# Kernel tuning notes

Hardware: AMD Instinct MI355X
Metric: run time of the kernel (lower is better)

The kernel has to match this reference:

```python
import jax, jax.numpy as jnp
import numpy as np

STRIDE = 4; R = 3; LEVELS = 4; LAT = 128; RES = (384, 512); D_IN = 1110; T_EMB = 50

def _sincos_1d(d, pos):
    omega = np.arange(d // 2, dtype=np.float64) / (d / 2.0)
    omega = 1.0 / 10000 ** omega
    out = pos.reshape(-1)[:, None] * omega[None, :]
    return np.concatenate([np.sin(out), np.cos(out)], axis=1).astype(np.float32)

def _support(coords, r):
    # coords [B, N, 3] (t, x, y) -> [B, N, 2r+1, 2r+1, 3]; offsets only in x,y
    d = jnp.linspace(-r, r, 2 * r + 1, dtype=jnp.float32)
    g0, g1 = jnp.meshgrid(d, d, indexing='ij')
    delta = jnp.stack([jnp.zeros_like(g0), g0, g1], axis=-1)
    return coords[:, :, None, None, :] + delta[None, None]

def _trilinear(fmap, coords):
    # fmap [B, C, Dd, H, W]; coords [B, M, 3] = (t, x, y); border padding, align_corners=True
    B, C, Dd, H, W = fmap.shape
    t = jnp.clip(coords[..., 0], 0.0, Dd - 1)
    x = jnp.clip(coords[..., 1], 0.0, W - 1)
    y = jnp.clip(coords[..., 2], 0.0, H - 1)
    t0f = jnp.floor(t); x0f = jnp.floor(x); y0f = jnp.floor(y)
    wt = (t - t0f)[:, None, :]; wx = (x - x0f)[:, None, :]; wy = (y - y0f)[:, None, :]
    t0 = t0f.astype(jnp.int32); t1 = jnp.minimum(t0 + 1, Dd - 1)
    x0 = x0f.astype(jnp.int32); x1 = jnp.minimum(x0 + 1, W - 1)
    y0 = y0f.astype(jnp.int32); y1 = jnp.minimum(y0 + 1, H - 1)
    flat = fmap.reshape(B, C, Dd * H * W)
    def g(ti, yi, xi):
        idx = (ti * H + yi) * W + xi
        return jnp.take_along_axis(flat, idx[:, None, :], axis=2)  # [B, C, M]
    def bilin(ti):
        v00 = g(ti, y0, x0); v01 = g(ti, y0, x1); v10 = g(ti, y1, x0); v11 = g(ti, y1, x1)
        return (v00 * (1 - wy) * (1 - wx) + v01 * (1 - wy) * wx
                + v10 * wy * (1 - wx) + v11 * wy * wx)
    return bilin(t0) * (1 - wt) + bilin(t1) * wt

def _posenc(x, min_deg, max_deg):
    scales = 2.0 ** jnp.arange(min_deg, max_deg, dtype=jnp.float32)
    xb = (x[..., None, :] * scales[:, None]).reshape(x.shape[:-1] + (-1,))
    ff = jnp.sin(jnp.concatenate([xb, xb + 0.5 * jnp.pi], axis=-1))
    return jnp.concatenate([x, ff], axis=-1)

def _interp_time(emb, t):
    T0 = emb.shape[1]
    if t == T0:
        return emb
    sc = T0 / float(t)
    j = jnp.clip((jnp.arange(t, dtype=jnp.float32) + 0.5) * sc - 0.5, 0.0, T0 - 1)
    j0 = jnp.floor(j).astype(jnp.int32); j1 = jnp.minimum(j0 + 1, T0 - 1)
    w = (j - j0)[None, :, None]
    return emb[:, j0] * (1 - w) + emb[:, j1] * w

def setup_inputs():
    key = jax.random.key(0)
    ks = jax.random.split(key, 10)
    B, T, N, H, W = 1, 16, 128, RES[0], RES[1]
    video = jax.random.uniform(ks[0], (B, T, 3, H, W), jnp.float32) * 255.0
    fr = jax.random.randint(ks[1], (B, N), 0, T).astype(jnp.float32)
    cx = jax.random.uniform(ks[2], (B, N), jnp.float32) * (W - 1)
    cy = jax.random.uniform(ks[3], (B, N), jnp.float32) * (H - 1)
    queries = jnp.stack([fr, cx, cy], axis=-1)
    s = 0.02
    return {
        'video': video,
        'queries': queries,
        'fnet_w': jax.random.normal(ks[4], (LAT, 3, 4, 4), jnp.float32) * s,
        'fnet_b': jnp.zeros((LAT,), jnp.float32),
        'fc1_w': jax.random.normal(ks[5], (2401, 384), jnp.float32) * s,
        'fc1_b': jnp.zeros((384,), jnp.float32),
        'fc2_w': jax.random.normal(ks[6], (384, 256), jnp.float32) * s,
        'fc2_b': jnp.zeros((256,), jnp.float32),
        'up_w1': jax.random.normal(ks[7], (D_IN, 384), jnp.float32) * s,
        'up_b1': jnp.zeros((384,), jnp.float32),
        'up_w2': jax.random.normal(ks[8], (384, 4), jnp.float32) * s,
        'up_b2': jnp.zeros((4,), jnp.float32),
        'time_emb': jnp.asarray(_sincos_1d(D_IN, np.linspace(0, T_EMB - 1, T_EMB))[None]),
        'iters': 4,
    }

def reference(video, queries, fnet_w, fnet_b, fc1_w, fc1_b, fc2_w, fc2_b,
              up_w1, up_b1, up_w2, up_b2, time_emb, iters):
    B, T, C, H, W = video.shape
    N = queries.shape[1]
    video = 2.0 * (video / 255.0) - 1.0
    qf = queries[:, :, 0]            # queried frames (used as float t coordinate)
    qc = queries[..., 1:3] / STRIDE  # (x, y) in feature-map coords
    # --- encoder (stand-in conv), L2-normalize over channels ---
    f = jax.lax.conv_general_dilated(video.reshape(B * T, C, H, W), fnet_w,
                                     (STRIDE, STRIDE), 'VALID') + fnet_b[None, :, None, None]
    f = f / jnp.sqrt(jnp.maximum(jnp.sum(f * f, axis=1, keepdims=True), 1e-12))
    fmaps = f.reshape(B, T, LAT, H // STRIDE, W // STRIDE)
    # --- avg-pool pyramid ---
    pyr = [fmaps]
    for _ in range(LEVELS - 1):
        p = pyr[-1]
        pyr.append(p.reshape(B, T, LAT, p.shape[-2] // 2, 2, p.shape[-1] // 2, 2).mean(axis=(4, 6)))
    r = R; rr = 2 * r + 1
    # --- track support features per level: [B, N, rr, rr, LAT] ---
    tfs = []
    for i in range(LEVELS):
        sc = jnp.concatenate([qf[..., None], qc / (2.0 ** i)], axis=-1)  # [B,N,3]
        sp = _support(sc, r).reshape(B, N * rr * rr, 3)
        feat = _trilinear(pyr[i].transpose(0, 2, 1, 3, 4), sp)  # [B, LAT, N*rr*rr]
        tfs.append(feat.reshape(B, LAT, N, rr, rr).transpose(0, 2, 3, 4, 1))
    vis = jnp.zeros((B, T, N), jnp.float32)
    conf = jnp.zeros((B, T, N), jnp.float32)
    coords = jnp.broadcast_to(qc.reshape(B, 1, N, 2), (B, T, N, 2)).astype(jnp.float32)
    scale = jnp.array([RES[1], RES[0]], jnp.float32) / STRIDE
    te = _interp_time(time_emb, T)  # [1, T, D_IN]
    for _ in range(iters):
        coords = jax.lax.stop_gradient(coords)
        cflat = coords.reshape(B * T, N, 2)
        embs = []
        for i in range(LEVELS):
            fm = pyr[i]
            Hi, Wi = fm.shape[-2], fm.shape[-1]
            sc = jnp.concatenate([jnp.zeros_like(cflat[..., :1]), cflat / (2.0 ** i)], axis=-1)
            sp = _support(sc, r).reshape(B * T, N * rr * rr, 3)
            cf = _trilinear(fm.reshape(B * T, LAT, 1, Hi, Wi), sp)  # [B*T, LAT, N*rr*rr]
            cf = cf.reshape(B, T, LAT, N, rr, rr).transpose(0, 1, 3, 4, 5, 2)  # [B,T,N,rr,rr,LAT]
            cv = jnp.einsum('btnhwc,bnijc->btnhwij', cf, tfs[i]).reshape(B * T * N, rr * rr * rr * rr)
            e = jax.nn.gelu(cv @ fc1_w + fc1_b, approximate=False) @ fc2_w + fc2_b
            embs.append(e)
        corr = jnp.concatenate(embs, axis=-1).reshape(B, T, N, -1)  # [B,T,N,1024]
        rf = jnp.pad(coords[:, :-1] - coords[:, 1:], ((0, 0), (0, 1), (0, 0), (0, 0))) / scale
        rb = jnp.pad(coords[:, 1:] - coords[:, :-1], ((0, 0), (1, 0), (0, 0), (0, 0))) / scale
        pe = _posenc(jnp.concatenate([rf, rb], axis=-1), 0, 10)  # [B,T,N,84]
        x = jnp.concatenate([vis[..., None], conf[..., None], corr, pe], axis=-1)  # [B,T,N,1110]
        x = x.transpose(0, 2, 1, 3) + te[None]  # [B,N,T,1110]
        delta = jax.nn.gelu(x @ up_w1 + up_b1, approximate=False) @ up_w2 + up_b2  # [B,N,T,4]
        coords = coords + delta[..., :2].transpose(0, 2, 1, 3)
        vis = vis + delta[..., 2].transpose(0, 2, 1)
        conf = conf + delta[..., 3].transpose(0, 2, 1)
    return coords * float(STRIDE), jax.nn.sigmoid(vis), jax.nn.sigmoid(conf)
```

## Files before the change

### kernel.cpp

```cpp
#include <hip/hip_runtime.h>
#include <math.h>

#define T_FR   16
#define N_Q    128
#define NSUP   49
#define H0     96
#define W0     128
#define DIN    1110
#define ITERS  4
#define KCV    2560
#define KU     1152

typedef __attribute__((ext_vector_type(8))) short short8;
typedef __attribute__((ext_vector_type(4))) float f32x4;

__device__ __forceinline__ float geluf(float x) {
    return 0.5f * x * (1.0f + erff(x * 0.70710678118654752f));
}
__device__ __forceinline__ unsigned short f2bf(float f) {
    unsigned u = __float_as_uint(f);
    u += 0x7fff + ((u >> 16) & 1);
    return (unsigned short)(u >> 16);
}
__device__ __forceinline__ float bf2f(unsigned short s) {
    return __uint_as_float(((unsigned)s) << 16);
}

__global__ void k_te(const float* __restrict__ emb, float* __restrict__ te) {
    int i = blockIdx.x * 256 + threadIdx.x;
    if (i >= T_FR * DIN) return;
    int t = i / DIN, d = i - t * DIN;
    float j = ((float)t + 0.5f) * (50.0f / 16.0f) - 0.5f;
    j = fminf(fmaxf(j, 0.0f), 49.0f);
    float j0f = floorf(j);
    int j0 = (int)j0f;
    int j1 = min(j0 + 1, 49);
    float w = j - j0f;
    te[i] = emb[j0 * DIN + d] * (1.0f - w) + emb[j1 * DIN + d] * w;
}

__global__ void k_init(const float* __restrict__ q, float* __restrict__ coords,
                       float* __restrict__ vis, float* __restrict__ conf) {
    int r = blockIdx.x * 256 + threadIdx.x;
    if (r >= T_FR * N_Q) return;
    int n = r & 127;
    coords[r * 2 + 0] = q[n * 3 + 1] * 0.25f;
    coords[r * 2 + 1] = q[n * 3 + 2] * 0.25f;
    vis[r] = 0.0f;
    conf[r] = 0.0f;
}

__global__ void k_prep1(const float* __restrict__ w, unsigned short* __restrict__ wt) {
    int i = blockIdx.x * 256 + threadIdx.x;
    if (i >= 2401 * 384) return;
    int k = i / 384, n = i - k * 384;
    int p = k / 49, q = k - p * 49;
    wt[(size_t)n * KCV + q * 52 + p] = f2bf(w[i]);
}

__global__ void k_prep(const float* __restrict__ w, unsigned short* __restrict__ wt,
                       int K, int N, int Ka, int total) {
    int i = blockIdx.x * 256 + threadIdx.x;
    if (i >= total) return;
    int k = i / N, n = i - k * N;
    wt[(size_t)n * Ka + k] = f2bf(w[i]);
}

__global__ void k_prepc(const float* __restrict__ w, unsigned short* __restrict__ wc) {
    int i = blockIdx.x * 256 + threadIdx.x;
    if (i >= 128 * 64) return;
    int ch = i >> 6, k = i & 63;
    wc[i] = (k < 48) ? f2bf(w[ch * 48 + k]) : (unsigned short)0;
}

#define APAD 72
__global__ __launch_bounds__(256) void k_conv(const float* __restrict__ video,
                                              const unsigned short* __restrict__ wc,
                                              const float* __restrict__ b,
                                              unsigned short* __restrict__ out) {
    __shared__ __align__(16) short As[128 * APAD];
    __shared__ __align__(16) short Bs[128 * APAD];
    const int y = blockIdx.x;
    const int tf = blockIdx.y;
    const int tid = threadIdx.x;

    {
        int pos = tid >> 1, half = tid & 1;
        short8 z = (short8){0,0,0,0,0,0,0,0};
        *(short8*)&As[pos * APAD + 48 + half * 8] = z;
    }
    #pragma unroll
    for (int s = 0; s < 6; ++s) {
        int chunk = s * 256 + tid;
        int c = chunk >> 9, r = chunk & 511;
        int ky = r >> 7, pos = r & 127;
        float4 v = *(const float4*)&video[(((size_t)(tf * 3 + c) * 384) + 4 * y + ky) * 512 + pos * 4];
        unsigned short o[4];
        o[0] = f2bf(v.x * (2.0f / 255.0f) - 1.0f);
        o[1] = f2bf(v.y * (2.0f / 255.0f) - 1.0f);
        o[2] = f2bf(v.z * (2.0f / 255.0f) - 1.0f);
        o[3] = f2bf(v.w * (2.0f / 255.0f) - 1.0f);
        *(uint2*)&As[pos * APAD + c * 16 + ky * 4] = *(const uint2*)o;
    }
    #pragma unroll
    for (int s = 0; s < 4; ++s) {
        int chunk = s * 256 + tid;
        int row = chunk >> 3, q = chunk & 7;
        *(uint4*)&Bs[row * APAD + q * 8] = *(const uint4*)&wc[row * 64 + q * 8];
    }
    __syncthreads();

    const int w = tid >> 6, lane = tid & 63, ml = lane & 15, quad = lane >> 4;
    f32x4 acc[2][8];
    #pragma unroll
    for (int mi = 0; mi < 2; ++mi)
        #pragma unroll
        for (int ni = 0; ni < 8; ++ni) acc[mi][ni] = (f32x4){0.f, 0.f, 0.f, 0.f};
    #pragma unroll
    for (int kk = 0; kk < 2; ++kk) {
        short8 af[2];
        #pragma unroll
        for (int mi = 0; mi < 2; ++mi)
            af[mi] = *(const short8*)&As[(w * 32 + mi * 16 + ml) * APAD + kk * 32 + quad * 8];
        #pragma unroll
        for (int ni = 0; ni < 8; ++ni) {
            short8 bv = *(const short8*)&Bs[(ni * 16 + ml) * APAD + kk * 32 + quad * 8];
            #pragma unroll
            for (int mi = 0; mi < 2; ++mi)
                acc[mi][ni] = __builtin_amdgcn_mfma_f32_16x16x32_bf16(af[mi], bv, acc[mi][ni], 0, 0, 0);
        }
    }
    float bias[8];
    #pragma unroll
    for (int ni = 0; ni < 8; ++ni) bias[ni] = b[ni * 16 + ml];
    unsigned short* obase = out + ((size_t)(tf * 96 + y) * 128) * 128;
    #pragma unroll
    for (int mi = 0; mi < 2; ++mi) {
        float s2[4];
        #pragma unroll
        for (int reg = 0; reg < 4; ++reg) {
            float s = 0.f;
            #pragma unroll
            for (int ni = 0; ni < 8; ++ni) {
                float v = acc[mi][ni][reg] + bias[ni];
                s = fmaf(v, v, s);
            }
            s += __shfl_xor(s, 1); s += __shfl_xor(s, 2);
            s += __shfl_xor(s, 4); s += __shfl_xor(s, 8);
            s2[reg] = rsqrtf(fmaxf(s, 1e-12f));
        }
        #pragma unroll
        for (int reg = 0; reg < 4; ++reg) {
            int pos = w * 32 + mi * 16 + quad * 4 + reg;
            #pragma unroll
            for (int ni = 0; ni < 8; ++ni)
                obase[(size_t)pos * 128 + ni * 16 + ml] = f2bf((acc[mi][ni][reg] + bias[ni]) * s2[reg]);
        }
    }
}

__global__ void k_pool(const unsigned short* __restrict__ in, unsigned short* __restrict__ out,
                       int Ho, int Wo, int total8) {
    int i = blockIdx.x * 256 + threadIdx.x;
    if (i >= total8) return;
    int c8 = i & 15;
    int rest = i >> 4;
    int x = rest % Wo; rest /= Wo;
    int y = rest % Ho;
    int bt = rest / Ho;
    int Wi = Wo * 2;
    const unsigned short* base = in + (size_t)bt * (Ho * 2) * Wi * 128;
    const unsigned short* p00 = base + ((size_t)(2 * y) * Wi + 2 * x) * 128 + c8 * 8;
    const unsigned short* p10 = base + ((size_t)(2 * y + 1) * Wi + 2 * x) * 128 + c8 * 8;
    unsigned short o[8];
    #pragma unroll
    for (int k = 0; k < 8; ++k)
        o[k] = f2bf(0.25f * (bf2f(p00[k]) + bf2f(p00[128 + k]) + bf2f(p10[k]) + bf2f(p10[128 + k])));
    unsigned short* dst = out + (size_t)i * 8;
    *(uint4*)dst = *(const uint4*)o;
}

__global__ __launch_bounds__(256) void k_template(const float* __restrict__ q,
    const unsigned short* __restrict__ p0, const unsigned short* __restrict__ p1,
    const unsigned short* __restrict__ p2, const unsigned short* __restrict__ p3,
    unsigned short* __restrict__ tfs) {
    __shared__ float gw[NSUP * 4];
    __shared__ int go[NSUP * 4];
    const int lvl = blockIdx.x >> 7;
    const int n = blockIdx.x & 127;
    const int tid = threadIdx.x;
    const unsigned short* fm; int Hi, Wi;
    if (lvl == 0)      { fm = p0; Hi = 96; Wi = 128; }
    else if (lvl == 1) { fm = p1; Hi = 48; Wi = 64; }
    else if (lvl == 2) { fm = p2; Hi = 24; Wi = 32; }
    else               { fm = p3; Hi = 12; Wi = 16; }
    float t = fminf(fmaxf(q[n * 3 + 0], 0.0f), (float)(T_FR - 1));
    float t0f = floorf(t);
    float wt = t - t0f;
    int t0 = (int)t0f, t1 = min(t0 + 1, T_FR - 1);
    if (tid < NSUP) {
        float inv = 1.0f / (float)(1 << lvl);
        float x = fminf(fmaxf(q[n * 3 + 1] * 0.25f * inv + (float)(tid / 7 - 3), 0.0f), (float)(Wi - 1));
        float y = fminf(fmaxf(q[n * 3 + 2] * 0.25f * inv + (float)(tid % 7 - 3), 0.0f), (float)(Hi - 1));
        float x0f = floorf(x), y0f = floorf(y);
        float wx = x - x0f, wy = y - y0f;
        int x0 = (int)x0f, y0 = (int)y0f;
        int x1 = min(x0 + 1, Wi - 1), y1 = min(y0 + 1, Hi - 1);
        gw[tid * 4 + 0] = (1 - wy) * (1 - wx);
        gw[tid * 4 + 1] = (1 - wy) * wx;
        gw[tid * 4 + 2] = wy * (1 - wx);
        gw[tid * 4 + 3] = wy * wx;
        go[tid * 4 + 0] = (y0 * Wi + x0) * 128;
        go[tid * 4 + 1] = (y0 * Wi + x1) * 128;
        go[tid * 4 + 2] = (y1 * Wi + x0) * 128;
        go[tid * 4 + 3] = (y1 * Wi + x1) * 128;
    }
    __syncthreads();
    size_t fs = (size_t)Hi * Wi * 128;
    const unsigned short* f0 = fm + (size_t)t0 * fs;
    const unsigned short* f1 = fm + (size_t)t1 * fs;
    unsigned short* obase = tfs + ((size_t)lvl * N_Q + n) * 64 * 128;
    #pragma unroll
    for (int s = 0; s < 4; ++s) {
        int i = s * 256 + tid;
        int p = i >> 4, c8 = i & 15;
        unsigned short o[8];
        if (p >= NSUP) {
            uint4 z = {0, 0, 0, 0};
            *(uint4*)&obase[(size_t)p * 128 + c8 * 8] = z;
            continue;
        }
        int o0 = go[p * 4 + 0] + c8 * 8, o1 = go[p * 4 + 1] + c8 * 8;
        int o2 = go[p * 4 + 2] + c8 * 8, o3 = go[p * 4 + 3] + c8 * 8;
        float w0 = gw[p * 4 + 0], w1 = gw[p * 4 + 1], w2 = gw[p * 4 + 2], w3 = gw[p * 4 + 3];
        uint4 a0 = *(const uint4*)&f0[o0], a1 = *(const uint4*)&f0[o1];
        uint4 a2 = *(const uint4*)&f0[o2], a3 = *(const uint4*)&f0[o3];
        uint4 b0 = *(const uint4*)&f1[o0], b1 = *(const uint4*)&f1[o1];
        uint4 b2 = *(const uint4*)&f1[o2], b3 = *(const uint4*)&f1[o3];
        const unsigned short* s0 = (const unsigned short*)&a0;
        const unsigned short* s1 = (const unsigned short*)&a1;
        const unsigned short* s2 = (const unsigned short*)&a2;
        const unsigned short* s3 = (const unsigned short*)&a3;
        const unsigned short* r0 = (const unsigned short*)&b0;
        const unsigned short* r1 = (const unsigned short*)&b1;
        const unsigned short* r2 = (const unsigned short*)&b2;
        const unsigned short* r3 = (const unsigned short*)&b3;
        #pragma unroll
        for (int j = 0; j < 8; ++j) {
            float v0 = w0 * bf2f(s0[j]) + w1 * bf2f(s1[j]) + w2 * bf2f(s2[j]) + w3 * bf2f(s3[j]);
            float v1 = w0 * bf2f(r0[j]) + w1 * bf2f(r1[j]) + w2 * bf2f(r2[j]) + w3 * bf2f(r3[j]);
            o[j] = f2bf(v0 * (1 - wt) + v1 * wt);
        }
        *(uint4*)&obase[(size_t)p * 128 + c8 * 8] = *(const uint4*)o;
    }
}

#define CPAD 136
__global__ __launch_bounds__(256) void k_corr(
    const unsigned short* __restrict__ p0, const unsigned short* __restrict__ p1,
    const unsigned short* __restrict__ p2, const unsigned short* __restrict__ p3,
    const unsigned short* __restrict__ tfs, const float* __restrict__ coords,
    unsigned short* __restrict__ cv) {
    __shared__ __align__(16) short tf_s[64 * CPAD];
    __shared__ __align__(16) short cf_s[64 * CPAD];
    __shared__ float gw[NSUP * 4];
    __shared__ int go[NSUP * 4];
    const int id = blockIdx.x;
    const int xcd = id & 7;
    const int j = id >> 3;
    const int lvl = j >> 8;
    const int bt = ((j >> 7) & 1) * 8 + xcd;
    const int n = j & 127;
    const int r = lvl * 2048 + bt * 128 + n;
    const int tid = threadIdx.x;

    const unsigned short* tsrc = tfs + ((size_t)lvl * N_Q + n) * 64 * 128;
    #pragma unroll
    for (int s = 0; s < 4; ++s) {
        int ch = s * 256 + tid;
        int row = ch >> 4, c8 = ch & 15;
        *(uint4*)&tf_s[row * CPAD + c8 * 8] = *(const uint4*)&tsrc[row * 128 + c8 * 8];
    }
    if (tid < 240) {
        int row = NSUP + tid / 16, c8 = tid % 16;
        uint4 z = {0, 0, 0, 0};
        *(uint4*)&cf_s[row * CPAD + c8 * 8] = z;
    }

    const unsigned short* fm; int Hi, Wi;
    if (lvl == 0)      { fm = p0; Hi = 96; Wi = 128; }
    else if (lvl == 1) { fm = p1; Hi = 48; Wi = 64; }
    else if (lvl == 2) { fm = p2; Hi = 24; Wi = 32; }
    else               { fm = p3; Hi = 12; Wi = 16; }
    if (tid < NSUP) {
        float inv = 1.0f / (float)(1 << lvl);
        float cx = coords[((size_t)bt * N_Q + n) * 2 + 0] * inv;
        float cy = coords[((size_t)bt * N_Q + n) * 2 + 1] * inv;
        float x = fminf(fmaxf(cx + (float)(tid / 7 - 3), 0.0f), (float)(Wi - 1));
        float y = fminf(fmaxf(cy + (float)(tid % 7 - 3), 0.0f), (float)(Hi - 1));
        float x0f = floorf(x), y0f = floorf(y);
        float wx = x - x0f, wy = y - y0f;
        int x0 = (int)x0f, y0 = (int)y0f;
        int x1 = min(x0 + 1, Wi - 1), y1 = min(y0 + 1, Hi - 1);
        gw[tid * 4 + 0] = (1 - wy) * (1 - wx);
        gw[tid * 4 + 1] = (1 - wy) * wx;
        gw[tid * 4 + 2] = wy * (1 - wx);
        gw[tid * 4 + 3] = wy * wx;
        go[tid * 4 + 0] = (y0 * Wi + x0) * 128;
        go[tid * 4 + 1] = (y0 * Wi + x1) * 128;
        go[tid * 4 + 2] = (y1 * Wi + x0) * 128;
        go[tid * 4 + 3] = (y1 * Wi + x1) * 128;
    }
    __syncthreads();

    const unsigned short* fbase = fm + (size_t)bt * Hi * Wi * 128;
    for (int i = tid; i < NSUP * 16; i += 256) {
        int p = i >> 4, c8 = i & 15;
        int o0 = go[p * 4 + 0] + c8 * 8, o1 = go[p * 4 + 1] + c8 * 8;
        int o2 = go[p * 4 + 2] + c8 * 8, o3 = go[p * 4 + 3] + c8 * 8;
        float w0 = gw[p * 4 + 0], w1 = gw[p * 4 + 1], w2 = gw[p * 4 + 2], w3 = gw[p * 4 + 3];
        uint4 a0 = *(const uint4*)&fbase[o0], a1 = *(const uint4*)&fbase[o1];
        uint4 a2 = *(const uint4*)&fbase[o2], a3 = *(const uint4*)&fbase[o3];
        const unsigned short* s0 = (const unsigned short*)&a0;
        const unsigned short* s1 = (const unsigned short*)&a1;
        const unsigned short* s2 = (const unsigned short*)&a2;
        const unsigned short* s3 = (const unsigned short*)&a3;
        unsigned short o[8];
        #pragma unroll
        for (int jj = 0; jj < 8; ++jj)
            o[jj] = f2bf(w0 * bf2f(s0[jj]) + w1 * bf2f(s1[jj]) + w2 * bf2f(s2[jj]) + w3 * bf2f(s3[jj]));
        *(uint4*)&cf_s[p * CPAD + c8 * 8] = *(const uint4*)o;
    }
    __syncthreads();

    const int w = tid >> 6, lane = tid & 63, ml = lane & 15, quad = lane >> 4;
    f32x4 acc[4];
    #pragma unroll
    for (int ni = 0; ni < 4; ++ni) acc[ni] = (f32x4){0.f, 0.f, 0.f, 0.f};
    #pragma unroll
    for (int kk = 0; kk < 4; ++kk) {
        short8 a = *(const short8*)&cf_s[(w * 16 + ml) * CPAD + kk * 32 + quad * 8];
        #pragma unroll
        for (int ni = 0; ni < 4; ++ni) {
            short8 b = *(const short8*)&tf_s[(ni * 16 + ml) * CPAD + kk * 32 + quad * 8];
            acc[ni] = __builtin_amdgcn_mfma_f32_16x16x32_bf16(a, b, acc[ni], 0, 0, 0);
        }
    }
    unsigned short* crow = cv + (size_t)r * KCV;
    const int p_base = w * 16 + quad * 4;
    #pragma unroll
    for (int ni = 0; ni < 4; ++ni) {
        int q = ni * 16 + ml;
        if (q < NSUP && p_base < 52) {
            unsigned short o4[4];
            #pragma unroll
            for (int reg = 0; reg < 4; ++reg) o4[reg] = f2bf(acc[ni][reg]);
            *(uint2*)&crow[q * 52 + p_base] = *(const uint2*)o4;
        }
    }
    if (tid < 12) crow[2548 + tid] = 0;
}

__global__ __launch_bounds__(256) void k_gdb(const unsigned short* __restrict__ A,
                                             const unsigned short* __restrict__ Wt,
                                             const float* __restrict__ bias,
                                             void* __restrict__ Cout,
                                             const float* __restrict__ te,
                                             int Ka, int nbn, int nbm, int ldc, int mode) {
    __shared__ __align__(16) short As[2][64 * 32];
    __shared__ __align__(16) short Bs[2][64 * 32];
    const int id = blockIdx.x;
    const int xcd = id & 7;
    const int j = id >> 3;
    const int mpx = nbm >> 3;
    const int m_blk = xcd * mpx + j / nbn;
    const int n_blk = j % nbn;
    const int gm0 = m_blk * 64, n0 = n_blk * 64;
    const int tid = threadIdx.x;
    const int w = tid >> 6, lane = tid & 63, ml = lane & 15, quad = lane >> 4;
    const int wm = w >> 1, wn = w & 1;
    const int sm = tid >> 2, sq = tid & 3;
    const int soff = sm * 32 + sq * 8;

    f32x4 acc[2][2];
    #pragma unroll
    for (int mi = 0; mi < 2; ++mi)
        #pragma unroll
        for (int ni = 0; ni < 2; ++ni) acc[mi][ni] = (f32x4){0.f, 0.f, 0.f, 0.f};

    const unsigned short* gA = A + (size_t)(gm0 + sm) * Ka + sq * 8;
    const unsigned short* gB = Wt + (size_t)(n0 + sm) * Ka + sq * 8;

    {
        uint4 ra = *(const uint4*)gA;
        uint4 rb = *(const uint4*)gB;
        *(uint4*)&As[0][soff] = ra;
        *(uint4*)&Bs[0][soff] = rb;
    }
    __syncthreads();

    const int nsteps = Ka >> 5;
    int cur = 0;
    for (int s = 0; s < nsteps; ++s) {
        uint4 ra, rb;
        if (s + 1 < nsteps) {
            ra = *(const uint4*)(gA + (s + 1) * 32);
            rb = *(const uint4*)(gB + (s + 1) * 32);
        }
        short8 af[2], bfr[2];
        #pragma unroll
        for (int mi = 0; mi < 2; ++mi)
            af[mi] = *(const short8*)&As[cur][(wm * 32 + mi * 16 + ml) * 32 + quad * 8];
        #pragma unroll
        for (int ni = 0; ni < 2; ++ni)
            bfr[ni] = *(const short8*)&Bs[cur][(wn * 32 + ni * 16 + ml) * 32 + quad * 8];
        #pragma unroll
        for (int mi = 0; mi < 2; ++mi)
            #pragma unroll
            for (int ni = 0; ni < 2; ++ni)
                acc[mi][ni] = __builtin_amdgcn_mfma_f32_16x16x32_bf16(af[mi], bfr[ni], acc[mi][ni], 0, 0, 0);
        if (s + 1 < nsteps) {
            __syncthreads();
            *(uint4*)&As[cur ^ 1][soff] = ra;
            *(uint4*)&Bs[cur ^ 1][soff] = rb;
            __syncthreads();
            cur ^= 1;
        }
    }

    #pragma unroll
    for (int mi = 0; mi < 2; ++mi) {
        #pragma unroll
        for (int ni = 0; ni < 2; ++ni) {
            int gn = n0 + wn * 32 + ni * 16 + ml;
            float bv = bias[gn];
            #pragma unroll
            for (int reg = 0; reg < 4; ++reg) {
                int gm = gm0 + wm * 32 + mi * 16 + quad * 4 + reg;
                float v = acc[mi][ni][reg] + bv;
                if (mode == 1) v = geluf(v);
                if (mode == 2) {
                    int row = gm & 2047, lvl = gm >> 11;
                    int d = 2 + lvl * 256 + gn;
                    int t = row >> 7;
                    ((unsigned short*)Cout)[(size_t)row * KU + d] = f2bf(v + te[t * DIN + d]);
                } else {
                    ((unsigned short*)Cout)[(size_t)gm * ldc + gn] = f2bf(v);
                }
            }
        }
    }
}

__global__ __launch_bounds__(128) void k_assemble(const float* __restrict__ coords,
                           const float* __restrict__ vis, const float* __restrict__ conf,
                           const float* __restrict__ te, unsigned short* __restrict__ x) {
    int r = blockIdx.x;
    int tid = threadIdx.x;
    int d = (tid < 2) ? tid : 1024 + tid;
    int t = r >> 7, n = r & 127;
    if (d >= DIN) { x[(size_t)r * KU + d] = 0; return; }
    float v;
    if (d == 0) v = vis[r];
    else if (d == 1) v = conf[r];
    else {
        int dd = d - 1026;
        float c0x = coords[r * 2], c0y = coords[r * 2 + 1];
        float v4[4];
        if (t < T_FR - 1) {
            v4[0] = (c0x - coords[((t + 1) * N_Q + n) * 2 + 0]) * (1.0f / 128.0f);
            v4[1] = (c0y - coords[((t + 1) * N_Q + n) * 2 + 1]) * (1.0f / 96.0f);
        } else { v4[0] = 0.f; v4[1] = 0.f; }
        if (t > 0) {
            v4[2] = (c0x - coords[((t - 1) * N_Q + n) * 2 + 0]) * (1.0f / 128.0f);
            v4[3] = (c0y - coords[((t - 1) * N_Q + n) * 2 + 1]) * (1.0f / 96.0f);
        } else { v4[2] = 0.f; v4[3] = 0.f; }
        if (dd < 4) v = v4[dd];
        else if (dd < 44) { int s = (dd - 4) >> 2, k = (dd - 4) & 3; v = sinf(v4[k] * (float)(1 << s)); }
        else              { int s = (dd - 44) >> 2, k = (dd - 44) & 3; v = cosf(v4[k] * (float)(1 << s)); }
    }
    x[(size_t)r * KU + d] = f2bf(v + te[t * DIN + d]);
}

__global__ __launch_bounds__(256) void k_up2(const unsigned short* __restrict__ h1,
                                             const float* __restrict__ w2,
                                             const float* __restrict__ b2,
                                             float* __restrict__ coords,
                                             float* __restrict__ vis,
                                             float* __restrict__ conf) {
    const int w = threadIdx.x >> 6, lane = threadIdx.x & 63;
    const int r = blockIdx.x * 4 + w;
    float a0 = 0.f, a1 = 0.f, a2 = 0.f, a3 = 0.f;
    if (lane < 48) {
        short8 av = *(const short8*)&h1[(size_t)r * 384 + lane * 8];
        const float* wp = w2 + lane * 32;
        #pragma unroll
        for (int j = 0; j < 8; ++j) {
            float x = bf2f((unsigned short)av[j]);
            a0 = fmaf(x, wp[j * 4 + 0], a0);
            a1 = fmaf(x, wp[j * 4 + 1], a1);
            a2 = fmaf(x, wp[j * 4 + 2], a2);
            a3 = fmaf(x, wp[j * 4 + 3], a3);
        }
    }
    #pragma unroll
    for (int m = 32; m > 0; m >>= 1) {
        a0 += __shfl_xor(a0, m); a1 += __shfl_xor(a1, m);
        a2 += __shfl_xor(a2, m); a3 += __shfl_xor(a3, m);
    }
    if (lane == 0) {
        coords[r * 2 + 0] += a0 + b2[0];
        coords[r * 2 + 1] += a1 + b2[1];
        vis[r] += a2 + b2[2];
        conf[r] += a3 + b2[3];
    }
}

__global__ void k_output(const float* __restrict__ coords, const float* __restrict__ vis,
                         const float* __restrict__ conf, float* __restrict__ out) {
    int r = blockIdx.x * 256 + threadIdx.x;
    if (r >= T_FR * N_Q) return;
    out[r * 2 + 0] = coords[r * 2 + 0] * 4.0f;
    out[r * 2 + 1] = coords[r * 2 + 1] * 4.0f;
    out[4096 + r] = 1.0f / (1.0f + expf(-vis[r]));
    out[6144 + r] = 1.0f / (1.0f + expf(-conf[r]));
}

extern "C" void kernel_launch(void* const* d_in, const int* in_sizes, int n_in,
                              void* d_out, int out_size, void* d_ws, size_t ws_size,
                              hipStream_t stream) {
    const float* video   = (const float*)d_in[0];
    const float* queries = (const float*)d_in[1];
    const float* fnet_w  = (const float*)d_in[2];
    const float* fnet_b  = (const float*)d_in[3];
    const float* fc1_w   = (const float*)d_in[4];
    const float* fc1_b   = (const float*)d_in[5];
    const float* fc2_w   = (const float*)d_in[6];
    const float* fc2_b   = (const float*)d_in[7];
    const float* up_w1   = (const float*)d_in[8];
    const float* up_b1   = (const float*)d_in[9];
    const float* up_w2   = (const float*)d_in[10];
    const float* up_b2   = (const float*)d_in[11];
    const float* t_emb   = (const float*)d_in[12];

    char* wsb = (char*)d_ws;
    size_t off = 0;
    #define ALLOC_US(name, elems) unsigned short* name = (unsigned short*)(wsb + off); off += ((size_t)(elems) * 2 + 15) & ~15ull;
    #define ALLOC_F(name, elems)  float* name = (float*)(wsb + off); off += ((size_t)(elems) * 4 + 15) & ~15ull;
    ALLOC_US(pyr0, (size_t)16 * 96 * 128 * 128)
    ALLOC_US(pyr1, (size_t)16 * 48 * 64 * 128)
    ALLOC_US(pyr2, (size_t)16 * 24 * 32 * 128)
    ALLOC_US(pyr3, (size_t)16 * 12 * 16 * 128)
    ALLOC_US(tfs,  (size_t)4 * N_Q * 64 * 128)
    ALLOC_US(cv,   (size_t)8192 * KCV)
    ALLOC_US(h1,   (size_t)8192 * 384)
    ALLOC_US(xb,   (size_t)2048 * KU)
    ALLOC_US(wt1,  (size_t)384 * KCV)
    ALLOC_US(wt2,  (size_t)256 * 384)
    ALLOC_US(wtu,  (size_t)384 * KU)
    ALLOC_US(wcv,  (size_t)128 * 64)
    ALLOC_F(te,   (size_t)T_FR * DIN)
    ALLOC_F(crd,  (size_t)2048 * 2)
    ALLOC_F(vis,  2048)
    ALLOC_F(conf, 2048)

    k_te<<<(T_FR * DIN + 255) / 256, 256, 0, stream>>>(t_emb, te);
    k_init<<<8, 256, 0, stream>>>(queries, crd, vis, conf);
    hipMemsetAsync(wt1, 0, (size_t)384 * KCV * 2, stream);
    k_prep1<<<(2401 * 384 + 255) / 256, 256, 0, stream>>>(fc1_w, wt1);
    k_prep<<<(384 * 256 + 255) / 256, 256, 0, stream>>>(fc2_w, wt2, 384, 256, 384, 384 * 256);
    k_prep<<<(DIN * 384 + 255) / 256, 256, 0, stream>>>(up_w1, wtu, DIN, 384, KU, DIN * 384);
    k_prepc<<<32, 256, 0, stream>>>(fnet_w, wcv);
    k_conv<<<dim3(96, 16), 256, 0, stream>>>(video, wcv, fnet_b, pyr0);
    k_pool<<<(16 * 48 * 64 * 16 + 255) / 256, 256, 0, stream>>>(pyr0, pyr1, 48, 64, 16 * 48 * 64 * 16);
    k_pool<<<(16 * 24 * 32 * 16 + 255) / 256, 256, 0, stream>>>(pyr1, pyr2, 24, 32, 16 * 24 * 32 * 16);
    k_pool<<<(16 * 12 * 16 * 16 + 255) / 256, 256, 0, stream>>>(pyr2, pyr3, 12, 16, 16 * 12 * 16 * 16);
    k_template<<<4 * N_Q, 256, 0, stream>>>(queries, pyr0, pyr1, pyr2, pyr3, tfs);

    for (int it = 0; it < ITERS; ++it) {
        k_corr<<<8192, 256, 0, stream>>>(pyr0, pyr1, pyr2, pyr3, tfs, crd, cv);
        k_gdb<<<768, 256, 0, stream>>>(cv, wt1, fc1_b, h1, nullptr, KCV, 6, 128, 384, 1);
        k_assemble<<<2048, 128, 0, stream>>>(crd, vis, conf, te, xb);
        k_gdb<<<512, 256, 0, stream>>>(h1, wt2, fc2_b, xb, te, 384, 4, 128, 0, 2);
        k_gdb<<<192, 256, 0, stream>>>(xb, wtu, up_b1, h1, nullptr, KU, 6, 32, 384, 1);
        k_up2<<<512, 256, 0, stream>>>(h1, up_w2, up_b2, crd, vis, conf);
    }
    k_output<<<8, 256, 0, stream>>>(crd, vis, conf, (float*)d_out);
}
```

Measured before the change: 612.9 us.

## Replace fc1 GEMM with 128x128 split-K kernel using async LDS loads

Swaps the 64x64 double-buffered GEMM for the large fc1 layer (8192x384x2560) for a 128x128-tile kernel that splits K four ways and stages tiles with global_load_lds direct-to-LDS copies. The fp32 partial sums go to a workspace and a separate reduction kernel adds bias, applies GELU and converts to bf16. The larger tiles raise operand reuse, but the kernel is single-buffered with two barriers per step, and the split-K path adds about 50MB of fp32 partial-sum traffic plus an extra launch.

New measurement: 619.6 us. Within noise of the previous version (+1.1%).

```diff
diff --git a/kernel.cpp b/kernel.cpp
--- a/kernel.cpp
+++ b/kernel.cpp
@@ -24,6 +24,11 @@
 }
 __device__ __forceinline__ float bf2f(unsigned short s) {
     return __uint_as_float(((unsigned)s) << 16);
+}
+__device__ __forceinline__ void async16(const void* g, void* l) {
+    __builtin_amdgcn_global_load_lds(
+        (const __attribute__((address_space(1))) void*)g,
+        (__attribute__((address_space(3))) void*)l, 16, 0, 0);
 }
 
 __global__ void k_te(const float* __restrict__ emb, float* __restrict__ te) {
@@ -361,6 +366,98 @@
     if (tid < 12) crow[2548 + tid] = 0;
 }
 
+__global__ __launch_bounds__(256) void k_ms128(const unsigned short* __restrict__ A,
+                                               const unsigned short* __restrict__ Wt,
+                                               float* __restrict__ Pbase,
+                                               int Ka, int nbn, int nbm, int N,
+                                               int nsteps, int S, int M) {
+    __shared__ __align__(16) short As[128 * 32];
+    __shared__ __align__(16) short Bs[128 * 32];
+    const int id = blockIdx.x;
+    const int xcd = id & 7;
+    const int j = id >> 3;
+    const int mpx = nbm >> 3;
+    const int sS = j % S;
+    const int jj = j / S;
+    const int n_blk = jj % nbn;
+    const int m_blk = xcd * mpx + jj / nbn;
+    const int gm0 = m_blk * 128, n0 = n_blk * 128;
+    const int kb = sS * (nsteps / S), ke = kb + nsteps / S;
+    const int tid = threadIdx.x;
+    const int w = tid >> 6, lane = tid & 63, ml = lane & 15, quad = lane >> 4;
+    const int wm = w >> 1, wn = w & 1;
+    const int wbase = (tid & 192) * 16;
+    f32x4 acc[4][4];
+    #pragma unroll
+    for (int mi = 0; mi < 4; ++mi)
+        #pragma unroll
+        for (int ni = 0; ni < 4; ++ni) acc[mi][ni] = (f32x4){0.f, 0.f, 0.f, 0.f};
+    const unsigned short* gA = A + (size_t)gm0 * Ka;
+    const unsigned short* gB = Wt + (size_t)n0 * Ka;
+    for (int k0 = kb * 32; k0 < ke * 32; k0 += 32) {
+        #pragma unroll
+        for (int ss = 0; ss < 2; ++ss) {
+            int chunk = ss * 256 + tid;
+            int m = chunk >> 2, q = chunk & 3;
+            async16(gA + (size_t)m * Ka + k0 + q * 8, (char*)As + ss * 4096 + wbase);
+        }
+        #pragma unroll
+        for (int ss = 0; ss < 2; ++ss) {
+            int chunk = ss * 256 + tid;
+            int m = chunk >> 2, q = chunk & 3;
+            async16(gB + (size_t)m * Ka + k0 + q * 8, (char*)Bs + ss * 4096 + wbase);
+        }
+        __syncthreads();
+        short8 af[4], bfr[4];
+        #pragma unroll
+        for (int mi = 0; mi < 4; ++mi)
+            af[mi] = *(const short8*)&As[(wm * 64 + mi * 16 + ml) * 32 + quad * 8];
+        #pragma unroll
+        for (int ni = 0; ni < 4; ++ni)
+            bfr[ni] = *(const short8*)&Bs[(wn * 64 + ni * 16 + ml) * 32 + quad * 8];
+        #pragma unroll
+        for (int mi = 0; mi < 4; ++mi)
+            #pragma unroll
+            for (int ni = 0; ni < 4; ++ni)
+                acc[mi][ni] = __builtin_amdgcn_mfma_f32_16x16x32_bf16(af[mi], bfr[ni], acc[mi][ni], 0, 0, 0);
+        __syncthreads();
+    }
+    float* P = Pbase + (size_t)sS * M * N;
+    #pragma unroll
+    for (int mi = 0; mi < 4; ++mi) {
+        #pragma unroll
+        for (int ni = 0; ni < 4; ++ni) {
+            int gn = n0 + wn * 64 + ni * 16 + ml;
+            #pragma unroll
+            for (int reg = 0; reg < 4; ++reg) {
+                int gm = gm0 + wm * 64 + mi * 16 + quad * 4 + reg;
+                P[(size_t)gm * N + gn] = acc[mi][ni][reg];
+            }
+        }
+    }
+}
+
+__global__ __launch_bounds__(256) void k_red(const float* __restrict__ P,
+                                             const float* __restrict__ bias,
+                                             unsigned short* __restrict__ out,
+                                             int MN4, int N4, int S) {
+    int i4 = blockIdx.x * 256 + threadIdx.x;
+    if (i4 >= MN4) return;
+    const float4* Pv = (const float4*)P;
+    float4 v = Pv[i4];
+    for (int s = 1; s < S; ++s) {
+        float4 u = Pv[(size_t)s * MN4 + i4];
+        v.x += u.x; v.y += u.y; v.z += u.z; v.w += u.w;
+    }
+    const float4 b = *(const float4*)&bias[(i4 % N4) * 4];
+    unsigned short o[4];
+    o[0] = f2bf(geluf(v.x + b.x));
+    o[1] = f2bf(geluf(v.y + b.y));
+    o[2] = f2bf(geluf(v.z + b.z));
+    o[3] = f2bf(geluf(v.w + b.w));
+    *(uint2*)&out[(size_t)i4 * 4] = *(const uint2*)o;
+}
+
 __global__ __launch_bounds__(256) void k_gdb(const unsigned short* __restrict__ A,
                                              const unsigned short* __restrict__ Wt,
                                              const float* __restrict__ bias,
@@ -559,6 +656,7 @@
     ALLOC_US(wt2,  (size_t)256 * 384)
     ALLOC_US(wtu,  (size_t)384 * KU)
     ALLOC_US(wcv,  (size_t)128 * 64)
+    ALLOC_F(pp,   (size_t)4 * 8192 * 384)
     ALLOC_F(te,   (size_t)T_FR * DIN)
     ALLOC_F(crd,  (size_t)2048 * 2)
     ALLOC_F(vis,  2048)
@@ -579,7 +677,8 @@
 
     for (int it = 0; it < ITERS; ++it) {
         k_corr<<<8192, 256, 0, stream>>>(pyr0, pyr1, pyr2, pyr3, tfs, crd, cv);
-        k_gdb<<<768, 256, 0, stream>>>(cv, wt1, fc1_b, h1, nullptr, KCV, 6, 128, 384, 1);
+        k_ms128<<<768, 256, 0, stream>>>(cv, wt1, pp, KCV, 3, 64, 384, 80, 4, 8192);
+        k_red<<<3072, 256, 0, stream>>>(pp, fc1_b, h1, 8192 * 96, 96, 4);
         k_assemble<<<2048, 128, 0, stream>>>(crd, vis, conf, te, xb);
         k_gdb<<<512, 256, 0, stream>>>(h1, wt2, fc2_b, xb, te, 384, 4, 128, 0, 2);
         k_gdb<<<192, 256, 0, stream>>>(xb, wtu, up_b1, h1, nullptr, KU, 6, 32, 384, 1);
```
